# Optimization experiments

Hardware: AMD Instinct MI355X
Metric: run time of the kernel (lower is better)

The kernel has to match this reference:

```python
import jax, jax.numpy as jnp
import numpy as np

B, S, D = 1, 4096, 1024
H, HKV, HD = 16, 4, 64          # q heads, kv heads, head dim
ROPE_THETA = 1e6


def setup_inputs() -> dict:
    key = jax.random.key(0)
    k1, k2, k3 = jax.random.split(key, 3)
    x = jax.random.normal(k1, (B, S, D), dtype=jnp.float32)
    # deterministic RoPE tables: pos_cis = exp(i * t * theta^{-2j/hd})
    inv_freq = 1.0 / (ROPE_THETA ** (np.arange(0, HD, 2, dtype=np.float32) / HD))  # [HD//2]
    ang = np.arange(S, dtype=np.float32)[:, None] * inv_freq[None, :]              # [S, HD//2]
    pos_cos = jnp.asarray(np.cos(ang), dtype=jnp.float32)
    pos_sin = jnp.asarray(np.sin(ang), dtype=jnp.float32)
    w_qkv = jax.random.normal(k2, (D, (H + 2 * HKV) * HD), dtype=jnp.float32) * 0.02
    w_o = jax.random.normal(k3, (H * HD, D), dtype=jnp.float32) * 0.02
    return {"x": x, "pos_cos": pos_cos, "pos_sin": pos_sin, "w_qkv": w_qkv, "w_o": w_o}


def _rope(t, pos_cos, pos_sin):
    # t: [B, S, h, HD]; complex pairs are consecutive elements on last dim
    te, to = t[..., 0::2], t[..., 1::2]
    cos = pos_cos[None, :, None, :]
    sin = pos_sin[None, :, None, :]
    oe = te * cos - to * sin
    oo = te * sin + to * cos
    return jnp.stack([oe, oo], axis=-1).reshape(t.shape)


def reference(x, pos_cos, pos_sin, w_qkv, w_o):
    qkv = jnp.einsum("bsd,de->bse", x, w_qkv)  # fused QKV projection
    q = qkv[..., : H * HD].reshape(B, S, H, HD)
    k = qkv[..., H * HD : (H + HKV) * HD].reshape(B, S, HKV, HD)
    v = qkv[..., (H + HKV) * HD :].reshape(B, S, HKV, HD)
    q = _rope(q, pos_cos, pos_sin)
    k = _rope(k, pos_cos, pos_sin)
    # GQA: repeat kv heads to match q heads
    n_rep = H // HKV
    k = jnp.repeat(k, n_rep, axis=2)  # [B, S, H, HD]
    v = jnp.repeat(v, n_rep, axis=2)
    scale = 1.0 / jnp.sqrt(jnp.float32(HD))
    scores = jnp.einsum("bqhd,bkhd->bhqk", q, k) * scale  # [B, H, S, S]
    causal = jnp.tril(jnp.ones((S, S), dtype=bool))
    scores = jnp.where(causal[None, None], scores, jnp.float32(-1e9))
    attn = jax.nn.softmax(scores, axis=-1)
    out = jnp.einsum("bhqk,bkhd->bqhd", attn, v).reshape(B, S, H * HD)
    return jnp.einsum("bse,ed->bsd", out, w_o)
```

## Files before the change

### kernel.cpp

```cpp
#include <hip/hip_runtime.h>

#define S_LEN 4096
#define DMODEL 1024
#define NH 16
#define NKV 4
#define HDIM 64
#define NQKV 1536

typedef __attribute__((ext_vector_type(8))) short bfrag8;
typedef __attribute__((ext_vector_type(4))) float f32x4_t;

__device__ __forceinline__ unsigned short f2bf(float f) {
  unsigned int u = __builtin_bit_cast(unsigned int, f);
  return (unsigned short)((u + 0x7fffu + ((u >> 16) & 1u)) >> 16);
}

__device__ __forceinline__ unsigned int cvtpk_bf16(float lo, float hi) {
  unsigned int r;
  asm("v_cvt_pk_bf16_f32 %0, %1, %2" : "=v"(r) : "v"(lo), "v"(hi));
  return r;
}

__device__ __forceinline__ float fexp2(float x) {
  float r;
  asm("v_exp_f32 %0, %1" : "=v"(r) : "v"(x));
  return r;
}

__device__ __forceinline__ float fmax3(float a, float b, float c) {
  float r;
  asm("v_max3_f32 %0, %1, %2, %3" : "=v"(r) : "v"(a), "v"(b), "v"(c));
  return r;
}

typedef __attribute__((address_space(3))) unsigned char lds_uc;
typedef const __attribute__((address_space(1))) unsigned char glob_uc;
__device__ __forceinline__ void gl16(const void* g, void* l) {
  __builtin_amdgcn_global_load_lds((glob_uc*)g, (lds_uc*)l, 16, 0, 0);
}

__global__ void convert_bf16(const float* __restrict__ in, unsigned short* __restrict__ out, int n) {
  int idx = (blockIdx.x * 256 + threadIdx.x) * 4;
  if (idx < n) {
    float4 v = *reinterpret_cast<const float4*>(in + idx);
    out[idx + 0] = f2bf(v.x);
    out[idx + 1] = f2bf(v.y);
    out[idx + 2] = f2bf(v.z);
    out[idx + 3] = f2bf(v.w);
  }
}

__global__ void transpose_convert(const float* __restrict__ in, int ldin, long in_zstride,
                                  unsigned short* __restrict__ out, int ldout, long out_zstride,
                                  int R, int C) {
  __shared__ float tile[32][33];
  const float* inb = in + (size_t)blockIdx.z * in_zstride;
  unsigned short* outb = out + (size_t)blockIdx.z * out_zstride;
  int c0 = blockIdx.x * 32, r0 = blockIdx.y * 32;
  int tx = threadIdx.x, ty = threadIdx.y;
  for (int i = 0; i < 4; ++i) {
    int r = r0 + ty + i * 8;
    tile[ty + i * 8][tx] = inb[(size_t)r * ldin + c0 + tx];
  }
  __syncthreads();
  for (int i = 0; i < 4; ++i) {
    int c = c0 + ty + i * 8;
    outb[(size_t)c * ldout + r0 + tx] = f2bf(tile[tx][ty + i * 8]);
  }
}

__global__ void rope_kernel(const float* __restrict__ qkv,
                            const float* __restrict__ pcos, const float* __restrict__ psin,
                            unsigned short* __restrict__ Qh, unsigned short* __restrict__ Kh) {
  const float SCL = 0.125f * 1.44269504f;
  int s = blockIdx.x;
  int t = threadIdx.x;
  const float* row = qkv + (size_t)s * NQKV;
  for (int p = t; p < 640; p += 256) {
    int i = p & 31;
    float c = pcos[s * 32 + i], sn = psin[s * 32 + i];
    if (p < 512) {
      int h = p >> 5;
      float te = row[h * 64 + 2 * i], to = row[h * 64 + 2 * i + 1];
      size_t base = ((size_t)h * S_LEN + s) * 64;
      Qh[base + 2 * i]     = f2bf((te * c - to * sn) * SCL);
      Qh[base + 2 * i + 1] = f2bf((te * sn + to * c) * SCL);
    } else {
      int hk = (p - 512) >> 5;
      float te = row[1024 + hk * 64 + 2 * i], to = row[1024 + hk * 64 + 2 * i + 1];
      size_t base = ((size_t)hk * S_LEN + s) * 64;
      Kh[base + 2 * i]     = f2bf(te * c - to * sn);
      Kh[base + 2 * i + 1] = f2bf(te * sn + to * c);
    }
  }
}

__global__ __launch_bounds__(256) void gemm_bf16(
    const unsigned short* __restrict__ A,
    const unsigned short* __restrict__ Bt,
    float* __restrict__ C, int M, int N, int K) {
  __shared__ __align__(16) unsigned short As[64 * 32];
  __shared__ __align__(16) unsigned short Bs[128 * 32];
  int m0 = blockIdx.x * 64, n0 = blockIdx.y * 128;
  int t = threadIdx.x, lane = t & 63, wid = t >> 6;
  int wm = (wid >> 1) * 32, wn = (wid & 1) * 64;
  int fr = lane & 15, kb = lane >> 4;
  int srow = t >> 2, scol = (t & 3) * 8;
  const unsigned short* Ag  = A + (size_t)(m0 + srow) * K + scol;
  const unsigned short* Bg0 = Bt + (size_t)(n0 + srow) * K + scol;
  const unsigned short* Bg1 = Bt + (size_t)(n0 + 64 + srow) * K + scol;
  char* AsW  = (char*)As + wid * 1024;
  char* BsW0 = (char*)Bs + wid * 1024;
  char* BsW1 = (char*)Bs + 4096 + wid * 1024;

  f32x4_t acc[2][4];
#pragma unroll
  for (int r = 0; r < 2; ++r)
#pragma unroll
    for (int c = 0; c < 4; ++c) acc[r][c] = (f32x4_t){0.f, 0.f, 0.f, 0.f};

  for (int k0 = 0; k0 < K; k0 += 32) {
    __syncthreads();
    gl16(Ag + k0, AsW);
    gl16(Bg0 + k0, BsW0);
    gl16(Bg1 + k0, BsW1);
    __syncthreads();
    bfrag8 af[2], bfr[4];
#pragma unroll
    for (int rb = 0; rb < 2; ++rb)
      af[rb] = *reinterpret_cast<const bfrag8*>(&As[(wm + rb * 16 + fr) * 32 + kb * 8]);
#pragma unroll
    for (int cb = 0; cb < 4; ++cb)
      bfr[cb] = *reinterpret_cast<const bfrag8*>(&Bs[(wn + cb * 16 + fr) * 32 + kb * 8]);
#pragma unroll
    for (int rb = 0; rb < 2; ++rb)
#pragma unroll
      for (int cb = 0; cb < 4; ++cb)
        acc[rb][cb] = __builtin_amdgcn_mfma_f32_16x16x32_bf16(af[rb], bfr[cb], acc[rb][cb], 0, 0, 0);
  }
  int rowg = (lane >> 4) * 4, colg = lane & 15;
#pragma unroll
  for (int rb = 0; rb < 2; ++rb)
#pragma unroll
    for (int cb = 0; cb < 4; ++cb)
#pragma unroll
      for (int j = 0; j < 4; ++j) {
        int r = m0 + wm + rb * 16 + rowg + j;
        int c = n0 + wn + cb * 16 + colg;
        C[(size_t)r * N + c] = acc[rb][cb][j];
      }
}

__global__ __launch_bounds__(256) void flash_attn(
    const unsigned short* __restrict__ Qh,
    const unsigned short* __restrict__ Kh,
    const unsigned short* __restrict__ Vt,
    unsigned short* __restrict__ aout) {
  __shared__ __align__(16) char SMEM[18432];
  int bid = blockIdx.x;
  int head = bid & 15, hk = head >> 2;
  int qt = 127 - (bid >> 4);
  int qrow0 = qt * 32;
  int t = threadIdx.x, lane = t & 63, wid = t >> 6;
  int fr = lane & 15, kb = lane >> 4, rloc = kb * 4;
  char* Pw = SMEM + wid * 4096;
  int swz = (fr & 7) << 4;

  const unsigned short* Qbase = Qh + ((size_t)head * S_LEN + qrow0) * 64;
  bfrag8 qf[2][2];
  qf[0][0] = *reinterpret_cast<const bfrag8*>(Qbase + fr * 64 + kb * 8);
  qf[0][1] = *reinterpret_cast<const bfrag8*>(Qbase + fr * 64 + 32 + kb * 8);
  qf[1][0] = *reinterpret_cast<const bfrag8*>(Qbase + (16 + fr) * 64 + kb * 8);
  qf[1][1] = *reinterpret_cast<const bfrag8*>(Qbase + (16 + fr) * 64 + 32 + kb * 8);

  const unsigned short* Kt = Kh + (size_t)hk * S_LEN * 64;
  const unsigned short* Vb = Vt + (size_t)hk * 64 * S_LEN;
  int koff = fr * 64 + kb * 8;
  int voff = fr * S_LEN + kb * 8;

  float m_r[2] = {-1e30f, -1e30f}, l_r[2] = {0.f, 0.f};
  f32x4_t acc[2][4];
#pragma unroll
  for (int g = 0; g < 2; ++g)
#pragma unroll
    for (int dt = 0; dt < 4; ++dt) acc[g][dt] = (f32x4_t){0.f, 0.f, 0.f, 0.f};

  int ntt = (qrow0 + 95) / 64;
  int nf = (qrow0 >= 63) ? ((qrow0 - 63) / 64 + 1) : 0;
  int c0 = (wid * ntt) >> 2, c1 = ((wid + 1) * ntt) >> 2;

  if (c0 < c1) {
    bfrag8 kf[4][2];
    {
      const unsigned short* K0 = Kt + c0 * 64 * 64 + koff;
#pragma unroll
      for (int ct = 0; ct < 4; ++ct) {
        kf[ct][0] = *reinterpret_cast<const bfrag8*>(K0 + ct * 1024);
        kf[ct][1] = *reinterpret_cast<const bfrag8*>(K0 + ct * 1024 + 32);
      }
    }
    for (int kt = c0; kt < c1; ++kt) {
      int kv0 = kt * 64;
      const unsigned short* Vtile = Vb + kv0 + voff;
      bfrag8 vf[2][4];
#pragma unroll
      for (int hh = 0; hh < 2; ++hh)
#pragma unroll
        for (int dt = 0; dt < 4; ++dt)
          vf[hh][dt] = *reinterpret_cast<const bfrag8*>(Vtile + dt * 16 * S_LEN + hh * 32);
      __builtin_amdgcn_sched_barrier(0);
      f32x4_t sc[2][4];
      __builtin_amdgcn_s_setprio(1);
#pragma unroll
      for (int ct = 0; ct < 4; ++ct) {
        f32x4_t z0 = (f32x4_t){0.f, 0.f, 0.f, 0.f};
        z0 = __builtin_amdgcn_mfma_f32_16x16x32_bf16(kf[ct][0], qf[0][0], z0, 0, 0, 0);
        sc[0][ct] = __builtin_amdgcn_mfma_f32_16x16x32_bf16(kf[ct][1], qf[0][1], z0, 0, 0, 0);
        f32x4_t z1 = (f32x4_t){0.f, 0.f, 0.f, 0.f};
        z1 = __builtin_amdgcn_mfma_f32_16x16x32_bf16(kf[ct][0], qf[1][0], z1, 0, 0, 0);
        sc[1][ct] = __builtin_amdgcn_mfma_f32_16x16x32_bf16(kf[ct][1], qf[1][1], z1, 0, 0, 0);
      }
      __builtin_amdgcn_s_setprio(0);
      if (kt + 1 < c1) {
        const unsigned short* Kn = Kt + (kv0 + 64) * 64 + koff;
#pragma unroll
        for (int ct = 0; ct < 4; ++ct) {
          kf[ct][0] = *reinterpret_cast<const bfrag8*>(Kn + ct * 1024);
          kf[ct][1] = *reinterpret_cast<const bfrag8*>(Kn + ct * 1024 + 32);
        }
      }
      __builtin_amdgcn_sched_barrier(0);
      if (kt >= nf) {
#pragma unroll
        for (int g = 0; g < 2; ++g) {
          int grow = qrow0 + g * 16 + fr;
#pragma unroll
          for (int ct = 0; ct < 4; ++ct)
#pragma unroll
            for (int j = 0; j < 4; ++j)
              sc[g][ct][j] = ((kv0 + ct * 16 + kb * 4 + j) <= grow) ? sc[g][ct][j] : -1e30f;
        }
      }
      float pmax[2];
#pragma unroll
      for (int g = 0; g < 2; ++g) {
        float pm = fmax3(sc[g][0][0], sc[g][0][1], sc[g][0][2]);
        pm = fmax3(pm, sc[g][0][3], sc[g][1][0]);
        pm = fmax3(pm, sc[g][1][1], sc[g][1][2]);
        pm = fmax3(pm, sc[g][1][3], sc[g][2][0]);
        pm = fmax3(pm, sc[g][2][1], sc[g][2][2]);
        pm = fmax3(pm, sc[g][2][3], sc[g][3][0]);
        pm = fmax3(pm, sc[g][3][1], sc[g][3][2]);
        pm = fmaxf(pm, sc[g][3][3]);
        pm = fmaxf(pm, __shfl_xor(pm, 16));
        pmax[g] = fmaxf(pm, __shfl_xor(pm, 32));
      }
      bool need = (pmax[0] > m_r[0] + 8.0f) || (pmax[1] > m_r[1] + 8.0f);
      if (__any(need)) {
#pragma unroll
        for (int g = 0; g < 2; ++g) {
          float mnew = fmaxf(m_r[g], pmax[g]);
          float a = fexp2(m_r[g] - mnew);
          l_r[g] *= a;
          m_r[g] = mnew;
#pragma unroll
          for (int j = 0; j < 4; ++j) {
            float aj = __shfl(a, rloc + j);
#pragma unroll
            for (int dt = 0; dt < 4; ++dt) acc[g][dt][j] *= aj;
          }
        }
      }
#pragma unroll
      for (int g = 0; g < 2; ++g) {
        float st[4];
#pragma unroll
        for (int ct = 0; ct < 4; ++ct) {
          float p0 = fexp2(sc[g][ct][0] - m_r[g]);
          float p1 = fexp2(sc[g][ct][1] - m_r[g]);
          float p2 = fexp2(sc[g][ct][2] - m_r[g]);
          float p3 = fexp2(sc[g][ct][3] - m_r[g]);
          sc[g][ct][0] = p0; sc[g][ct][1] = p1; sc[g][ct][2] = p2; sc[g][ct][3] = p3;
          st[ct] = (p0 + p1) + (p2 + p3);
        }
        l_r[g] += (st[0] + st[1]) + (st[2] + st[3]);
      }
#pragma unroll
      for (int g = 0; g < 2; ++g)
#pragma unroll
        for (int ct = 0; ct < 4; ++ct) {
          unsigned int u01 = cvtpk_bf16(sc[g][ct][0], sc[g][ct][1]);
          unsigned int u23 = cvtpk_bf16(sc[g][ct][2], sc[g][ct][3]);
          unsigned long long w = ((unsigned long long)u23 << 32) | u01;
          *reinterpret_cast<unsigned long long*>(
              Pw + (g * 16 + fr) * 128 + ((ct * 32 + kb * 8) ^ swz)) = w;
        }
      __builtin_amdgcn_s_setprio(1);
#pragma unroll
      for (int hh = 0; hh < 2; ++hh) {
        bfrag8 pa0 = *reinterpret_cast<const bfrag8*>(Pw + fr * 128 + ((hh * 64 + kb * 16) ^ swz));
        bfrag8 pa1 = *reinterpret_cast<const bfrag8*>(Pw + (16 + fr) * 128 + ((hh * 64 + kb * 16) ^ swz));
#pragma unroll
        for (int dt = 0; dt < 4; ++dt) {
          acc[0][dt] = __builtin_amdgcn_mfma_f32_16x16x32_bf16(pa0, vf[hh][dt], acc[0][dt], 0, 0, 0);
          acc[1][dt] = __builtin_amdgcn_mfma_f32_16x16x32_bf16(pa1, vf[hh][dt], acc[1][dt], 0, 0, 0);
        }
      }
      __builtin_amdgcn_s_setprio(0);
    }
  }

  float* stgA = (float*)SMEM;
  float* stgB = (float*)(SMEM + 9216);
  __syncthreads();
  if (wid == 1 || wid == 3) {
    float* R = (wid == 1) ? stgA : stgB;
#pragma unroll
    for (int g = 0; g < 2; ++g) {
#pragma unroll
      for (int dt = 0; dt < 4; ++dt)
#pragma unroll
        for (int j = 0; j < 4; ++j)
          R[(g * 16 + dt * 4 + j) * 64 + lane] = acc[g][dt][j];
      R[(32 + g * 2) * 64 + lane] = m_r[g];
      R[(33 + g * 2) * 64 + lane] = l_r[g];
    }
  }
  __syncthreads();
  if (wid == 0 || wid == 2) {
    float* R = (wid == 0) ? stgA : stgB;
#pragma unroll
    for (int g = 0; g < 2; ++g) {
      float mo = R[(32 + g * 2) * 64 + lane], lo = R[(33 + g * 2) * 64 + lane];
      float mm = fmaxf(m_r[g], mo);
      float ca = fexp2(m_r[g] - mm), cb = fexp2(mo - mm);
      l_r[g] = l_r[g] * ca + lo * cb;
      m_r[g] = mm;
#pragma unroll
      for (int j = 0; j < 4; ++j) {
        float caj = __shfl(ca, rloc + j);
        float cbj = __shfl(cb, rloc + j);
#pragma unroll
        for (int dt = 0; dt < 4; ++dt)
          acc[g][dt][j] = acc[g][dt][j] * caj + R[(g * 16 + dt * 4 + j) * 64 + lane] * cbj;
      }
    }
    if (wid == 2) {
#pragma unroll
      for (int g = 0; g < 2; ++g) {
#pragma unroll
        for (int dt = 0; dt < 4; ++dt)
#pragma unroll
          for (int j = 0; j < 4; ++j)
            stgB[(g * 16 + dt * 4 + j) * 64 + lane] = acc[g][dt][j];
        stgB[(32 + g * 2) * 64 + lane] = m_r[g];
        stgB[(33 + g * 2) * 64 + lane] = l_r[g];
      }
    }
  }
  __syncthreads();
  if (wid == 0) {
#pragma unroll
    for (int g = 0; g < 2; ++g) {
      float mo = stgB[(32 + g * 2) * 64 + lane], lo = stgB[(33 + g * 2) * 64 + lane];
      float mm = fmaxf(m_r[g], mo);
      float ca = fexp2(m_r[g] - mm), cb = fexp2(mo - mm);
      l_r[g] = l_r[g] * ca + lo * cb;
#pragma unroll
      for (int j = 0; j < 4; ++j) {
        float caj = __shfl(ca, rloc + j);
        float cbj = __shfl(cb, rloc + j);
#pragma unroll
        for (int dt = 0; dt < 4; ++dt)
          acc[g][dt][j] = acc[g][dt][j] * caj + stgB[(g * 16 + dt * 4 + j) * 64 + lane] * cbj;
      }
    }
#pragma unroll
    for (int g = 0; g < 2; ++g) {
      l_r[g] += __shfl_xor(l_r[g], 16);
      l_r[g] += __shfl_xor(l_r[g], 32);
    }
#pragma unroll
    for (int g = 0; g < 2; ++g)
#pragma unroll
      for (int j = 0; j < 4; ++j) {
        float lj = __shfl(l_r[g], rloc + j);
        float inv = 1.0f / lj;
        int grow = qrow0 + g * 16 + rloc + j;
#pragma unroll
        for (int dt = 0; dt < 4; ++dt)
          aout[(size_t)grow * (NH * HDIM) + head * 64 + dt * 16 + fr] = f2bf(acc[g][dt][j] * inv);
      }
  }
}

extern "C" void kernel_launch(void* const* d_in, const int* in_sizes, int n_in,
                              void* d_out, int out_size, void* d_ws, size_t ws_size,
                              hipStream_t stream) {
  const float* x    = (const float*)d_in[0];
  const float* pcos = (const float*)d_in[1];
  const float* psin = (const float*)d_in[2];
  const float* wqkv = (const float*)d_in[3];
  const float* wo   = (const float*)d_in[4];
  float* out = (float*)d_out;

  char* ws = (char*)d_ws;
  unsigned short* xb    = (unsigned short*)ws;  ws += (size_t)S_LEN * DMODEL * 2;
  unsigned short* wqkvT = (unsigned short*)ws;  ws += (size_t)NQKV * DMODEL * 2;
  unsigned short* woT   = (unsigned short*)ws;  ws += (size_t)DMODEL * DMODEL * 2;
  float*          qkv   = (float*)ws;           ws += (size_t)S_LEN * NQKV * 4;
  unsigned short* Qh    = (unsigned short*)ws;  ws += (size_t)NH * S_LEN * HDIM * 2;
  unsigned short* Kh    = (unsigned short*)ws;  ws += (size_t)NKV * S_LEN * HDIM * 2;
  unsigned short* Vt    = (unsigned short*)ws;  ws += (size_t)NKV * HDIM * S_LEN * 2;
  unsigned short* aoutb = (unsigned short*)ws;  ws += (size_t)S_LEN * NH * HDIM * 2;

  convert_bf16<<<(S_LEN * DMODEL) / (256 * 4), 256, 0, stream>>>(x, xb, S_LEN * DMODEL);
  transpose_convert<<<dim3(NQKV / 32, DMODEL / 32, 1), dim3(32, 8), 0, stream>>>(
      wqkv, NQKV, 0, wqkvT, DMODEL, 0, DMODEL, NQKV);
  transpose_convert<<<dim3(DMODEL / 32, DMODEL / 32, 1), dim3(32, 8), 0, stream>>>(
      wo, DMODEL, 0, woT, DMODEL, 0, DMODEL, DMODEL);
  gemm_bf16<<<dim3(S_LEN / 64, NQKV / 128), 256, 0, stream>>>(xb, wqkvT, qkv, S_LEN, NQKV, DMODEL);
  rope_kernel<<<S_LEN, 256, 0, stream>>>(qkv, pcos, psin, Qh, Kh);
  transpose_convert<<<dim3(HDIM / 32, S_LEN / 32, NKV), dim3(32, 8), 0, stream>>>(
      qkv + 1280, NQKV, 64, Vt, S_LEN, (long)HDIM * S_LEN, S_LEN, HDIM);
  flash_attn<<<dim3(2048), 256, 0, stream>>>(Qh, Kh, Vt, aoutb);
  gemm_bf16<<<dim3(S_LEN / 64, DMODEL / 128), 256, 0, stream>>>(aoutb, woT, out, S_LEN, DMODEL, DMODEL);
}
```

Baseline: 196.0 us.

## Merge preprocessing and rope/V-transpose launches, double GEMM K tile

Folds the x conversion and both weight transpose-converts into one preprocess launch, and the RoPE and V transpose into one rope_vt launch, so there are fewer kernel launches and gaps between them. The bf16 GEMM now stages a K slice of 64 per iteration instead of 32, which halves the number of barrier pairs per tile in exchange for doubling LDS use. The merged kernels branch on block index, so their blocks do uneven amounts of work.

```diff
diff --git a/kernel.cpp b/kernel.cpp
--- a/kernel.cpp
+++ b/kernel.cpp
@@ -39,59 +39,94 @@
   __builtin_amdgcn_global_load_lds((glob_uc*)g, (lds_uc*)l, 16, 0, 0);
 }
 
-__global__ void convert_bf16(const float* __restrict__ in, unsigned short* __restrict__ out, int n) {
-  int idx = (blockIdx.x * 256 + threadIdx.x) * 4;
-  if (idx < n) {
-    float4 v = *reinterpret_cast<const float4*>(in + idx);
-    out[idx + 0] = f2bf(v.x);
-    out[idx + 1] = f2bf(v.y);
-    out[idx + 2] = f2bf(v.z);
-    out[idx + 3] = f2bf(v.w);
-  }
-}
-
-__global__ void transpose_convert(const float* __restrict__ in, int ldin, long in_zstride,
-                                  unsigned short* __restrict__ out, int ldout, long out_zstride,
-                                  int R, int C) {
+__global__ void preprocess(const float* __restrict__ x, const float* __restrict__ wqkv,
+                           const float* __restrict__ wo,
+                           unsigned short* __restrict__ xb, unsigned short* __restrict__ wqkvT,
+                           unsigned short* __restrict__ woT) {
   __shared__ float tile[32][33];
-  const float* inb = in + (size_t)blockIdx.z * in_zstride;
-  unsigned short* outb = out + (size_t)blockIdx.z * out_zstride;
-  int c0 = blockIdx.x * 32, r0 = blockIdx.y * 32;
-  int tx = threadIdx.x, ty = threadIdx.y;
+  int b = blockIdx.x;
+  int t = threadIdx.x;
+  if (b < 4096) {
+    int idx = (b * 256 + t) * 4;
+    float4 v = *reinterpret_cast<const float4*>(x + idx);
+    xb[idx + 0] = f2bf(v.x);
+    xb[idx + 1] = f2bf(v.y);
+    xb[idx + 2] = f2bf(v.z);
+    xb[idx + 3] = f2bf(v.w);
+    return;
+  }
+  int tx = t & 31, ty = t >> 5;
+  const float* in;
+  unsigned short* out;
+  int ldin, ldout, c0, r0;
+  if (b < 4096 + 1536) {
+    int id = b - 4096;
+    c0 = (id % 48) * 32;
+    r0 = (id / 48) * 32;
+    in = wqkv; out = wqkvT; ldin = NQKV; ldout = DMODEL;
+  } else {
+    int id = b - 4096 - 1536;
+    c0 = (id & 31) * 32;
+    r0 = (id >> 5) * 32;
+    in = wo; out = woT; ldin = DMODEL; ldout = DMODEL;
+  }
   for (int i = 0; i < 4; ++i) {
     int r = r0 + ty + i * 8;
-    tile[ty + i * 8][tx] = inb[(size_t)r * ldin + c0 + tx];
+    tile[ty + i * 8][tx] = in[(size_t)r * ldin + c0 + tx];
   }
   __syncthreads();
   for (int i = 0; i < 4; ++i) {
     int c = c0 + ty + i * 8;
-    outb[(size_t)c * ldout + r0 + tx] = f2bf(tile[tx][ty + i * 8]);
-  }
-}
-
-__global__ void rope_kernel(const float* __restrict__ qkv,
-                            const float* __restrict__ pcos, const float* __restrict__ psin,
-                            unsigned short* __restrict__ Qh, unsigned short* __restrict__ Kh) {
-  const float SCL = 0.125f * 1.44269504f;
-  int s = blockIdx.x;
+    out[(size_t)c * ldout + r0 + tx] = f2bf(tile[tx][ty + i * 8]);
+  }
+}
+
+__global__ void rope_vt(const float* __restrict__ qkv,
+                        const float* __restrict__ pcos, const float* __restrict__ psin,
+                        unsigned short* __restrict__ Qh, unsigned short* __restrict__ Kh,
+                        unsigned short* __restrict__ Vt) {
+  int b = blockIdx.x;
   int t = threadIdx.x;
-  const float* row = qkv + (size_t)s * NQKV;
-  for (int p = t; p < 640; p += 256) {
-    int i = p & 31;
-    float c = pcos[s * 32 + i], sn = psin[s * 32 + i];
-    if (p < 512) {
-      int h = p >> 5;
-      float te = row[h * 64 + 2 * i], to = row[h * 64 + 2 * i + 1];
-      size_t base = ((size_t)h * S_LEN + s) * 64;
-      Qh[base + 2 * i]     = f2bf((te * c - to * sn) * SCL);
-      Qh[base + 2 * i + 1] = f2bf((te * sn + to * c) * SCL);
-    } else {
-      int hk = (p - 512) >> 5;
-      float te = row[1024 + hk * 64 + 2 * i], to = row[1024 + hk * 64 + 2 * i + 1];
-      size_t base = ((size_t)hk * S_LEN + s) * 64;
-      Kh[base + 2 * i]     = f2bf(te * c - to * sn);
-      Kh[base + 2 * i + 1] = f2bf(te * sn + to * c);
-    }
+  if (b < 4096) {
+    const float SCL = 0.125f * 1.44269504f;
+    int s = b;
+    const float* row = qkv + (size_t)s * NQKV;
+    for (int p = t; p < 640; p += 256) {
+      int i = p & 31;
+      float c = pcos[s * 32 + i], sn = psin[s * 32 + i];
+      if (p < 512) {
+        int h = p >> 5;
+        float te = row[h * 64 + 2 * i], to = row[h * 64 + 2 * i + 1];
+        size_t base = ((size_t)h * S_LEN + s) * 64;
+        Qh[base + 2 * i]     = f2bf((te * c - to * sn) * SCL);
+        Qh[base + 2 * i + 1] = f2bf((te * sn + to * c) * SCL);
+      } else {
+        int hk = (p - 512) >> 5;
+        float te = row[1024 + hk * 64 + 2 * i], to = row[1024 + hk * 64 + 2 * i + 1];
+        size_t base = ((size_t)hk * S_LEN + s) * 64;
+        Kh[base + 2 * i]     = f2bf(te * c - to * sn);
+        Kh[base + 2 * i + 1] = f2bf(te * sn + to * c);
+      }
+    }
+    return;
+  }
+  __shared__ float tile[32][33];
+  int id = b - 4096;
+  int dt = id & 1;
+  int st = (id >> 1) & 127;
+  int hk = id >> 8;
+  int tx = t & 31, ty = t >> 5;
+  const float* inb = qkv + 1280 + hk * 64 + dt * 32;
+  unsigned short* outb = Vt + (size_t)hk * HDIM * S_LEN + (size_t)dt * 32 * S_LEN;
+  int s0 = st * 32;
+  for (int i = 0; i < 4; ++i) {
+    int r = s0 + ty + i * 8;
+    tile[ty + i * 8][tx] = inb[(size_t)r * NQKV + tx];
+  }
+  __syncthreads();
+  for (int i = 0; i < 4; ++i) {
+    int d = ty + i * 8;
+    outb[(size_t)d * S_LEN + s0 + tx] = f2bf(tile[tx][d]);
   }
 }
 
@@ -99,19 +134,25 @@
     const unsigned short* __restrict__ A,
     const unsigned short* __restrict__ Bt,
     float* __restrict__ C, int M, int N, int K) {
-  __shared__ __align__(16) unsigned short As[64 * 32];
-  __shared__ __align__(16) unsigned short Bs[128 * 32];
+  __shared__ __align__(16) unsigned short As[64 * 64];
+  __shared__ __align__(16) unsigned short Bs[128 * 64];
   int m0 = blockIdx.x * 64, n0 = blockIdx.y * 128;
   int t = threadIdx.x, lane = t & 63, wid = t >> 6;
   int wm = (wid >> 1) * 32, wn = (wid & 1) * 64;
   int fr = lane & 15, kb = lane >> 4;
-  int srow = t >> 2, scol = (t & 3) * 8;
-  const unsigned short* Ag  = A + (size_t)(m0 + srow) * K + scol;
+  int srow = t >> 3, scol = (t & 7) * 8;
+  const unsigned short* Ag0 = A + (size_t)(m0 + srow) * K + scol;
+  const unsigned short* Ag1 = A + (size_t)(m0 + 32 + srow) * K + scol;
   const unsigned short* Bg0 = Bt + (size_t)(n0 + srow) * K + scol;
-  const unsigned short* Bg1 = Bt + (size_t)(n0 + 64 + srow) * K + scol;
-  char* AsW  = (char*)As + wid * 1024;
-  char* BsW0 = (char*)Bs + wid * 1024;
-  char* BsW1 = (char*)Bs + 4096 + wid * 1024;
+  const unsigned short* Bg1 = Bt + (size_t)(n0 + 32 + srow) * K + scol;
+  const unsigned short* Bg2 = Bt + (size_t)(n0 + 64 + srow) * K + scol;
+  const unsigned short* Bg3 = Bt + (size_t)(n0 + 96 + srow) * K + scol;
+  char* AsD0 = (char*)As + wid * 1024;
+  char* AsD1 = (char*)As + 4096 + wid * 1024;
+  char* BsD0 = (char*)Bs + wid * 1024;
+  char* BsD1 = (char*)Bs + 4096 + wid * 1024;
+  char* BsD2 = (char*)Bs + 8192 + wid * 1024;
+  char* BsD3 = (char*)Bs + 12288 + wid * 1024;
 
   f32x4_t acc[2][4];
 #pragma unroll
@@ -119,24 +160,33 @@
 #pragma unroll
     for (int c = 0; c < 4; ++c) acc[r][c] = (f32x4_t){0.f, 0.f, 0.f, 0.f};
 
-  for (int k0 = 0; k0 < K; k0 += 32) {
+  for (int k0 = 0; k0 < K; k0 += 64) {
     __syncthreads();
-    gl16(Ag + k0, AsW);
-    gl16(Bg0 + k0, BsW0);
-    gl16(Bg1 + k0, BsW1);
+    gl16(Ag0 + k0, AsD0);
+    gl16(Ag1 + k0, AsD1);
+    gl16(Bg0 + k0, BsD0);
+    gl16(Bg1 + k0, BsD1);
+    gl16(Bg2 + k0, BsD2);
+    gl16(Bg3 + k0, BsD3);
     __syncthreads();
-    bfrag8 af[2], bfr[4];
+    bfrag8 af[2][2], bfr[4][2];
 #pragma unroll
     for (int rb = 0; rb < 2; ++rb)
-      af[rb] = *reinterpret_cast<const bfrag8*>(&As[(wm + rb * 16 + fr) * 32 + kb * 8]);
+#pragma unroll
+      for (int h = 0; h < 2; ++h)
+        af[rb][h] = *reinterpret_cast<const bfrag8*>(&As[(wm + rb * 16 + fr) * 64 + h * 32 + kb * 8]);
 #pragma unroll
     for (int cb = 0; cb < 4; ++cb)
-      bfr[cb] = *reinterpret_cast<const bfrag8*>(&Bs[(wn + cb * 16 + fr) * 32 + kb * 8]);
+#pragma unroll
+      for (int h = 0; h < 2; ++h)
+        bfr[cb][h] = *reinterpret_cast<const bfrag8*>(&Bs[(wn + cb * 16 + fr) * 64 + h * 32 + kb * 8]);
 #pragma unroll
     for (int rb = 0; rb < 2; ++rb)
 #pragma unroll
-      for (int cb = 0; cb < 4; ++cb)
-        acc[rb][cb] = __builtin_amdgcn_mfma_f32_16x16x32_bf16(af[rb], bfr[cb], acc[rb][cb], 0, 0, 0);
+      for (int cb = 0; cb < 4; ++cb) {
+        acc[rb][cb] = __builtin_amdgcn_mfma_f32_16x16x32_bf16(af[rb][0], bfr[cb][0], acc[rb][cb], 0, 0, 0);
+        acc[rb][cb] = __builtin_amdgcn_mfma_f32_16x16x32_bf16(af[rb][1], bfr[cb][1], acc[rb][cb], 0, 0, 0);
+      }
   }
   int rowg = (lane >> 4) * 4, colg = lane & 15;
 #pragma unroll
@@ -414,15 +464,9 @@
   unsigned short* Vt    = (unsigned short*)ws;  ws += (size_t)NKV * HDIM * S_LEN * 2;
   unsigned short* aoutb = (unsigned short*)ws;  ws += (size_t)S_LEN * NH * HDIM * 2;
 
-  convert_bf16<<<(S_LEN * DMODEL) / (256 * 4), 256, 0, stream>>>(x, xb, S_LEN * DMODEL);
-  transpose_convert<<<dim3(NQKV / 32, DMODEL / 32, 1), dim3(32, 8), 0, stream>>>(
-      wqkv, NQKV, 0, wqkvT, DMODEL, 0, DMODEL, NQKV);
-  transpose_convert<<<dim3(DMODEL / 32, DMODEL / 32, 1), dim3(32, 8), 0, stream>>>(
-      wo, DMODEL, 0, woT, DMODEL, 0, DMODEL, DMODEL);
+  preprocess<<<dim3(4096 + 1536 + 1024), 256, 0, stream>>>(x, wqkv, wo, xb, wqkvT, woT);
   gemm_bf16<<<dim3(S_LEN / 64, NQKV / 128), 256, 0, stream>>>(xb, wqkvT, qkv, S_LEN, NQKV, DMODEL);
-  rope_kernel<<<S_LEN, 256, 0, stream>>>(qkv, pcos, psin, Qh, Kh);
-  transpose_convert<<<dim3(HDIM / 32, S_LEN / 32, NKV), dim3(32, 8), 0, stream>>>(
-      qkv + 1280, NQKV, 64, Vt, S_LEN, (long)HDIM * S_LEN, S_LEN, HDIM);
+  rope_vt<<<dim3(4096 + 1024), 256, 0, stream>>>(qkv, pcos, psin, Qh, Kh, Vt);
   flash_attn<<<dim3(2048), 256, 0, stream>>>(Qh, Kh, Vt, aoutb);
   gemm_bf16<<<dim3(S_LEN / 64, DMODEL / 128), 256, 0, stream>>>(aoutb, woT, out, S_LEN, DMODEL, DMODEL);
 }
```

New measurement: 189.3 us. 3.4% less time.
